# Performance work log

Hardware: AMD Instinct MI355X
Metric: run time of the kernel (lower is better)

The kernel has to match this reference:

```python
import jax, jax.numpy as jnp
import numpy as np
from jax import lax

B, N, C, P = 4, 20000, 21, 100           # batch, anchors, classes (incl. background), proposal_count
SCORE_THR = 0.7
SIGMA = 0.5                              # soft_nms=True -> soft_nms_sigma = 0.5
CLIP_RATIO = 16.0 / 1000.0
BIG = 1e9                                # sentinel for invalid / removed boxes
MAX_RATIO = float(abs(np.log(CLIP_RATIO)))


def setup_inputs() -> dict:
    key = jax.random.key(0)
    k1, k2, k3, k4, k5 = jax.random.split(key, 5)
    score = jax.random.uniform(k1, (B, N, 1), dtype=jnp.float32)
    logits = jax.random.uniform(k2, (B, N, C), dtype=jnp.float32)
    regress = jax.random.normal(k3, (B, N, 4), dtype=jnp.float32) * 0.2
    ctr = jax.random.uniform(k4, (N, 2), minval=0.05, maxval=0.95)
    size = jax.random.uniform(k5, (N, 2), minval=0.02, maxval=0.3)
    anchors = jnp.clip(jnp.concatenate([ctr - 0.5 * size, ctr + 0.5 * size], axis=-1), 0.0, 1.0)
    return {"score": score, "logits": logits, "regress": regress, "anchors": anchors.astype(jnp.float32)}


def _decode(anchors, regress):
    # delta2bbox-style decode (yolo2bbox) with wh-ratio clipping, boxes clipped to [0,1]
    ax1, ay1, ax2, ay2 = anchors[:, 0], anchors[:, 1], anchors[:, 2], anchors[:, 3]
    aw, ah = ax2 - ax1, ay2 - ay1
    acx, acy = ax1 + 0.5 * aw, ay1 + 0.5 * ah
    dx, dy = regress[:, 0], regress[:, 1]
    dw = jnp.clip(regress[:, 2], -MAX_RATIO, MAX_RATIO)
    dh = jnp.clip(regress[:, 3], -MAX_RATIO, MAX_RATIO)
    cx, cy = acx + dx * aw, acy + dy * ah
    w, h = aw * jnp.exp(dw), ah * jnp.exp(dh)
    boxes = jnp.stack([cx - 0.5 * w, cy - 0.5 * h, cx + 0.5 * w, cy + 0.5 * h], axis=-1)
    return jnp.clip(boxes, 0.0, 1.0)


def _iou_one(b, boxes):
    # IoU of one box [4] vs all boxes [N,4]
    x1 = jnp.maximum(b[0], boxes[:, 0])
    y1 = jnp.maximum(b[1], boxes[:, 1])
    x2 = jnp.minimum(b[2], boxes[:, 2])
    y2 = jnp.minimum(b[3], boxes[:, 3])
    inter = jnp.clip(x2 - x1, 0.0) * jnp.clip(y2 - y1, 0.0)
    a = (b[2] - b[0]) * (b[3] - b[1])
    areas = (boxes[:, 2] - boxes[:, 0]) * (boxes[:, 3] - boxes[:, 1])
    return inter / (a + areas - inter + 1e-9)


def _soft_nms(boxes, scores0):
    # Gaussian soft-NMS (TF non_max_suppression_with_scores, soft_nms_sigma>0):
    # weight = exp(-0.5*iou^2/sigma); iou_threshold is ignored in soft mode.
    n = scores0.shape[0]
    ar = jnp.arange(n)

    @jax.checkpoint
    def step(carry, _):
        s, removed = carry
        m = jnp.where(removed, -BIG, s)
        i = jnp.argmax(m)
        valid = m[i] > 0.0
        w = jnp.exp(-0.5 * jnp.square(_iou_one(boxes[i], boxes)) / SIGMA)
        s = jnp.where(valid, s * w, s)
        removed = removed | (ar == i)
        return (s, removed), (i, valid)

    _, (idx, val) = lax.scan(step, (scores0, jnp.zeros(n, bool)), None, length=P)
    return idx, val


def _image(score, logits, regress, anchors):
    le = score * logits                       # [N,C] combined class scores
    label = jnp.argmax(le, axis=-1)
    ms = jnp.max(le, axis=-1)
    valid = (ms >= SCORE_THR) & (label > 0)   # drop background / low score
    boxes = _decode(anchors, regress)         # [N,4]
    cls_scores = jnp.where(valid[None, :], le.T[1:], -BIG)   # [C-1,N]
    idx, val = jax.vmap(_soft_nms, in_axes=(None, 0))(boxes, cls_scores)  # [C-1,P]
    cls = jnp.broadcast_to(jnp.arange(1, C)[:, None], (C - 1, P))
    idx, val, cls = idx.reshape(-1), val.reshape(-1), cls.reshape(-1)
    cand = jnp.where(val, le[idx, cls], -BIG)  # gather_nd on un-decayed logit
    top_s, top_i = lax.top_k(cand, P)          # global top-k over all classes
    fi = idx[top_i]
    ok = (top_s > -BIG / 2)[:, None]
    logit_out = jnp.where(ok, le[fi], 0.0)     # zero-padded like tf.pad
    proposal = jnp.where(ok, boxes[fi], 0.0)
    return logit_out, proposal                 # [P,C], [P,4]


def reference(score, logits, regress, anchors):
    return jax.vmap(_image, in_axes=(0, 0, 0, None))(score, logits, regress, anchors)
```

## Files before the change

kernel.cpp:

```cpp
#include <hip/hip_runtime.h>
#include <climits>
#include <cstdint>

namespace {
constexpr int B = 4, N = 20000, C = 21, P = 100, NC = 20;
constexpr float THR  = 0.7f;
constexpr float BIGF = 1.0e9f;
constexpr float MAXR = 4.135166556742356f;
constexpr float TAU  = 0.8f;
constexpr int NMT  = 512;
constexpr int PCAP = NMT;
constexpr int TKN  = 2048;
constexpr int TKT  = 512;
constexpr int NB   = (N + 255) / 256;
constexpr int GPB  = 2;
constexpr int GB   = (NB + GPB - 1) / GPB;

constexpr size_t OFF_CPACK = 0;
constexpr size_t OFF_MASK  = OFF_CPACK + (size_t)B * N * 32;
constexpr size_t OFF_BCNT  = OFF_MASK  + (size_t)B * N * 4;
constexpr size_t OFF_VCNT  = OFF_BCNT  + 2048;
constexpr size_t OFF_OIDX  = OFF_VCNT  + 64;
constexpr size_t OFF_OVAL  = OFF_OIDX  + (size_t)B * NC * P * 4;
constexpr size_t OFF_OSC   = OFF_OVAL  + (size_t)B * NC * P * 4;
constexpr size_t OFF_OBOX  = OFF_OSC   + (size_t)B * NC * P * 4;
constexpr size_t OFF_SFALL = OFF_OBOX  + (size_t)B * NC * P * 16;
}

template <int CTRL, int RM>
__device__ __forceinline__ float dpp_fmax(float x) {
  int t = __builtin_amdgcn_update_dpp(__float_as_int(x), __float_as_int(x),
                                      CTRL, RM, 0xF, false);
  return fmaxf(x, __int_as_float(t));
}
__device__ __forceinline__ float wave_fmax64(float x) {
  x = dpp_fmax<0x111, 0xF>(x);
  x = dpp_fmax<0x112, 0xF>(x);
  x = dpp_fmax<0x114, 0xF>(x);
  x = dpp_fmax<0x118, 0xF>(x);
  x = dpp_fmax<0x142, 0xA>(x);
  x = dpp_fmax<0x143, 0xC>(x);
  return __int_as_float(__builtin_amdgcn_readlane(__float_as_int(x), 63));
}
__device__ __forceinline__ float fast_rcp(float x) {
  return __builtin_amdgcn_rcpf(x);
}
__device__ __forceinline__ float fast_exp2(float x) {
  return __builtin_amdgcn_exp2f(x);
}
__device__ __forceinline__ unsigned fmap(float v) {
  unsigned u = __float_as_uint(v);
  return (u & 0x80000000u) ? ~u : (u | 0x80000000u);
}
__device__ __forceinline__ float funmap(unsigned u) {
  return __uint_as_float((u & 0x80000000u) ? (u ^ 0x80000000u) : ~u);
}

__global__ __launch_bounds__(256) void k_valid(
    const float* __restrict__ score, const float* __restrict__ logits,
    unsigned* __restrict__ mask, int* __restrict__ bcnt) {
  __shared__ int ws[4];
  int tid = threadIdx.x;
  int n = blockIdx.x * 256 + tid;
  int b = blockIdx.y;
  unsigned mk = 0;
  if (n < N) {
    int bn = b * N + n;
    float sc = score[bn];
    const float* lg = logits + (size_t)bn * C;
    float le[C];
    float ms = -INFINITY;
    int lab = 0;
    #pragma unroll
    for (int c = 0; c < C; ++c) {
      le[c] = __fmul_rn(sc, lg[c]);
      if (le[c] > ms) { ms = le[c]; lab = c; }
    }
    if (ms >= THR && lab > 0) {
      mk = 1u << 20;
      #pragma unroll
      for (int c = 1; c < C; ++c)
        if (le[c] >= TAU) mk |= 1u << (c - 1);
    }
    mask[bn] = mk;
  }
  unsigned long long vb = __ballot(mk != 0);
  if ((tid & 63) == 0) ws[tid >> 6] = __popcll(vb);
  __syncthreads();
  if (tid == 0) bcnt[b * NB + blockIdx.x] = ws[0] + ws[1] + ws[2] + ws[3];
}

__global__ __launch_bounds__(256) void k_compact(
    const float* __restrict__ score, const float* __restrict__ regress,
    const float* __restrict__ anchors, const unsigned* __restrict__ mask,
    const int* __restrict__ bcnt, float* __restrict__ cpack,
    int* __restrict__ vcnt) {
  __shared__ int s_base[4], s_tot[4], s_scan[4];
  int g = blockIdx.x, b = blockIdx.y;
  int tid = threadIdx.x, lane = tid & 63, wid = tid >> 6;
  int idx0 = g * GPB;
  int bv = (tid < idx0) ? bcnt[b * NB + tid] : 0;
  int tv = (tid < NB) ? bcnt[b * NB + tid] : 0;
  #pragma unroll
  for (int off = 32; off; off >>= 1) {
    bv += __shfl_down(bv, off);
    tv += __shfl_down(tv, off);
  }
  if (lane == 0) { s_base[wid] = bv; s_tot[wid] = tv; }
  __syncthreads();
  int base = s_base[0] + s_base[1] + s_base[2] + s_base[3];
  if (g == 0 && tid == 0) vcnt[b] = s_tot[0] + s_tot[1] + s_tot[2] + s_tot[3];

  int n0 = g * (GPB * 256) + tid * GPB;
  unsigned bits = 0; int cnt = 0;
  #pragma unroll
  for (int j = 0; j < GPB; ++j) {
    int n = n0 + j;
    if (n < N && (mask[b * N + n] & (1u << 20))) { bits |= 1u << j; cnt++; }
  }
  int inc = cnt;
  #pragma unroll
  for (int off = 1; off < 64; off <<= 1) {
    int o = __shfl_up(inc, off);
    if (lane >= off) inc += o;
  }
  if (lane == 63) s_scan[wid] = inc;
  __syncthreads();
  int woff = 0;
  for (int k = 0; k < wid; ++k) woff += s_scan[k];
  int pos = base + woff + inc - cnt;
  #pragma unroll
  for (int j = 0; j < GPB; ++j) {
    if (!((bits >> j) & 1u)) continue;
    int n = n0 + j;
    int bn = b * N + n;
    const float* an = anchors + (size_t)n * 4;
    float ax1 = an[0], ay1 = an[1], ax2 = an[2], ay2 = an[3];
    float aw = __fsub_rn(ax2, ax1), ah = __fsub_rn(ay2, ay1);
    float acx = __fadd_rn(ax1, __fmul_rn(0.5f, aw));
    float acy = __fadd_rn(ay1, __fmul_rn(0.5f, ah));
    const float* rg = regress + (size_t)bn * 4;
    float dx = rg[0], dy = rg[1];
    float dw = fminf(fmaxf(rg[2], -MAXR), MAXR);
    float dh = fminf(fmaxf(rg[3], -MAXR), MAXR);
    float cx = __fadd_rn(acx, __fmul_rn(dx, aw));
    float cy = __fadd_rn(acy, __fmul_rn(dy, ah));
    float w = __fmul_rn(aw, expf(dw));
    float h = __fmul_rn(ah, expf(dh));
    float hw = __fmul_rn(0.5f, w), hh = __fmul_rn(0.5f, h);
    float x1 = fminf(fmaxf(__fsub_rn(cx, hw), 0.f), 1.f);
    float y1 = fminf(fmaxf(__fsub_rn(cy, hh), 0.f), 1.f);
    float x2 = fminf(fmaxf(__fadd_rn(cx, hw), 0.f), 1.f);
    float y2 = fminf(fmaxf(__fadd_rn(cy, hh), 0.f), 1.f);
    float area = __fmul_rn(__fsub_rn(x2, x1), __fsub_rn(y2, y1));
    unsigned mk = mask[bn];
    float4* cp = reinterpret_cast<float4*>(cpack) + ((size_t)b * N + pos) * 2;
    cp[0] = make_float4(x1, y1, x2, y2);
    cp[1] = make_float4(__int_as_float(n), score[bn], area, __uint_as_float(mk));
    pos++;
  }
}

__global__ __launch_bounds__(NMT) void k_nms(
    const float* __restrict__ logits, const float* __restrict__ cpack,
    const int* __restrict__ vcnt, float* __restrict__ sfall,
    int* __restrict__ oidx, int* __restrict__ oval,
    float* __restrict__ osc, float* __restrict__ obox) {
  constexpr int NW = NMT / 64;
  __shared__ float4 s_box[PCAP];
  __shared__ float  s_ar[PCAP], s_s[PCAP];
  __shared__ int    s_n[PCAP];
  __shared__ int    s_selj[P];
  __shared__ int    s_wcnt[NW];
  __shared__ int    s_fail;
  __shared__ unsigned long long s_gk[2];
  __shared__ float  s_red[NW];
  __shared__ int    s_redi[NW];

  int blk = blockIdx.x;
  int b = blk / NC;
  int cls = blk % NC + 1;
  int V = vcnt[b];
  int tid = threadIdx.x;
  int lane = tid & 63, wid = tid >> 6;
  const float* cpf = cpack + (size_t)b * N * 8;
  int* oi = oidx + (size_t)blk * P;
  int* ov = oval + (size_t)blk * P;
  float* os = osc + (size_t)blk * P;
  float4* ob = reinterpret_cast<float4*>(obox) + (size_t)blk * P;
  unsigned clsbit = 1u << (cls - 1);

  s_box[tid] = make_float4(0.f, 0.f, 0.f, 0.f);
  if (tid == 0) { s_gk[0] = 0ull; s_gk[1] = 0ull; }

  int ch = (V + NMT - 1) / NMT;
  int v0 = tid * ch, v1 = min(v0 + ch, V);
  int cnt = 0;
  for (int v = v0; v < v1; ++v) {
    unsigned mk = __float_as_uint(cpf[(size_t)v * 8 + 7]);
    if (mk & clsbit) cnt++;
  }
  int inc = cnt;
  #pragma unroll
  for (int off = 1; off < 64; off <<= 1) {
    int o = __shfl_up(inc, off);
    if (lane >= off) inc += o;
  }
  if (lane == 63) s_wcnt[wid] = inc;
  __syncthreads();
  int woff = 0;
  for (int k = 0; k < wid; ++k) woff += s_wcnt[k];
  int pcnt = 0;
  #pragma unroll
  for (int k = 0; k < NW; ++k) pcnt += s_wcnt[k];
  int pos = woff + inc - cnt;
  for (int v = v0; v < v1; ++v) {
    const float4* cp = reinterpret_cast<const float4*>(cpf) + (size_t)v * 2;
    float4 f2 = cp[1];
    unsigned mk = __float_as_uint(f2.w);
    if (mk & clsbit) {
      if (pos < PCAP) {
        float4 f1 = cp[0];
        int n = __float_as_int(f2.x);
        float lg = logits[(size_t)(b * N + n) * C + cls];
        s_s[pos]   = __fmul_rn(f2.y, lg);
        s_box[pos] = f1;
        s_ar[pos]  = f2.z;
        s_n[pos]   = n;
      }
      pos++;
    }
  }
  __syncthreads();

  bool fail0 = (pcnt > PCAP);
  if (!fail0) {
    bool in = tid < pcnt;
    float4 q = s_box[tid];
    float sr = in ? s_s[tid] : -INFINITY;
    float qx = q.x, qy = q.y, qz = q.z, qw = q.w;
    float pa = in ? s_ar[tid] : 0.f;
    unsigned long long kb = 0ull;

    for (int t = 0; t < P; ++t) {
      int par = t & 1;
      float lm = wave_fmax64(sr);
      unsigned long long bm = __ballot(sr == lm);
      int lane_w = __ffsll(bm) - 1;
      if (lane == 0) {
        unsigned inv = 511u - (unsigned)(wid * 64 + lane_w);
        unsigned long long key = ((unsigned long long)(t + 1) << 41) |
                                 ((unsigned long long)fmap(lm) << 9) |
                                 (unsigned long long)inv;
        atomicMax(&s_gk[par], key);
      }
      __syncthreads();
      kb = s_gk[par];
      int j_w = 511 - (int)((unsigned)kb & 511u);
      if (tid == 0) s_selj[t] = j_w;
      float4 wbx = s_box[j_w];
      float wa = __fmul_rn(__fsub_rn(wbx.z, wbx.x),
                           __fsub_rn(wbx.w, wbx.y));
      float s1 = __fadd_rn(wa, 1e-9f);
      float x1 = fmaxf(wbx.x, qx), y1 = fmaxf(wbx.y, qy);
      float x2 = fminf(wbx.z, qz), y2 = fminf(wbx.w, qw);
      float iw = fmaxf(__fsub_rn(x2, x1), 0.f);
      float ih = fmaxf(__fsub_rn(y2, y1), 0.f);
      float inter = __fmul_rn(iw, ih);
      float den = __fsub_rn(__fadd_rn(pa, s1), inter);
      float iou = __fmul_rn(inter, fast_rcp(den));
      float m2 = __fmul_rn(__fmul_rn(iou, iou), -1.44269504089f);
      float wgt = fast_exp2(m2);
      float ns = __fmul_rn(sr, wgt);
      sr = (tid == j_w) ? -INFINITY : ns;
    }
    float gmax = funmap((unsigned)((kb >> 9) & 0xFFFFFFFFull));
    if (tid == 0) s_fail = (gmax < TAU) ? 1 : 0;
    __syncthreads();
    if (!s_fail) {
      if (tid < P) {
        int wj = s_selj[tid];
        oi[tid] = s_n[wj];
        ov[tid] = 1;
        os[tid] = s_s[wj];
        ob[tid] = s_box[wj];
      }
      return;
    }
  }

  __syncthreads();
  float* sg = sfall + (size_t)blk * N;
  for (int v = tid; v < V; v += NMT) {
    const float* c2 = cpf + (size_t)v * 8 + 4;
    int n = __float_as_int(c2[0]);
    sg[v] = __fmul_rn(c2[1], logits[(size_t)(b * N + n) * C + cls]);
  }
  __syncthreads();

  for (int t = 0; t < P; ++t) {
    float bv = -INFINITY; int bi = INT_MAX;
    for (int v = tid; v < V; v += NMT) {
      float sv = sg[v];
      if (sv > bv) { bv = sv; bi = v; }
    }
    #pragma unroll
    for (int off = 32; off; off >>= 1) {
      float ovv = __shfl_down(bv, off); int oii = __shfl_down(bi, off);
      if (ovv > bv || (ovv == bv && oii < bi)) { bv = ovv; bi = oii; }
    }
    if (lane == 0) { s_red[wid] = bv; s_redi[wid] = bi; }
    __syncthreads();
    float wv = -INFINITY; int wi = INT_MAX;
    #pragma unroll
    for (int k = 0; k < NW; ++k) {
      float v = s_red[k]; int i = s_redi[k];
      if (v > wv || (v == wv && i < wi)) { wv = v; wi = i; }
    }
    __syncthreads();
    if (wi == INT_MAX) {
      if (tid == 0) for (int u = t; u < P; ++u) {
        oi[u] = 0; ov[u] = 0; os[u] = 0.f;
        ob[u] = make_float4(0.f, 0.f, 0.f, 0.f);
      }
      break;
    }
    int vd = (wv > 0.0f) ? 1 : 0;
    const float* cw = cpf + (size_t)wi * 8;
    if (tid == 0) {
      int n = __float_as_int(cw[4]);
      oi[t] = n; ov[t] = vd;
      os[t] = __fmul_rn(cw[5], logits[(size_t)(b * N + n) * C + cls]);
      ob[t] = make_float4(cw[0], cw[1], cw[2], cw[3]);
    }
    float w0, w1, w2, w3;
    if (vd) { w0 = cw[0]; w1 = cw[1]; w2 = cw[2]; w3 = cw[3]; }
    else    { w0 = w1 = w2 = w3 = 0.f; }
    float wa = __fmul_rn(__fsub_rn(w2, w0), __fsub_rn(w3, w1));
    for (int v = tid; v < V; v += NMT) {
      float sv = (v == wi) ? -INFINITY : sg[v];
      const float* cq = cpf + (size_t)v * 8;
      float x1 = fmaxf(w0, cq[0]), y1 = fmaxf(w1, cq[1]);
      float x2 = fminf(w2, cq[2]), y2 = fminf(w3, cq[3]);
      float iw = fmaxf(__fsub_rn(x2, x1), 0.f);
      float ih = fmaxf(__fsub_rn(y2, y1), 0.f);
      float inter = __fmul_rn(iw, ih);
      float den = __fadd_rn(__fsub_rn(__fadd_rn(wa, cq[6]), inter), 1e-9f);
      float iou = __fdiv_rn(inter, den);
      float wgt = expf(-__fmul_rn(iou, iou));
      sg[v] = __fmul_rn(sv, wgt);
    }
    __syncthreads();
  }
}

__global__ __launch_bounds__(TKT) void k_topk(
    const float* __restrict__ score, const float* __restrict__ logits,
    const float* __restrict__ obox, const int* __restrict__ oidx,
    const int* __restrict__ oval, const float* __restrict__ osc,
    float* __restrict__ out) {
  __shared__ unsigned long long s_k2[2][TKN];
  __shared__ int s_fi[TKN];

  int b = blockIdx.x;
  int tid = threadIdx.x;
  size_t base = (size_t)b * NC * P;

  unsigned long long v0, v1, v2, v3;
  {
    int j0 = 4 * tid;
    if (j0 + 3 < NC * P) {
      int4   vl4 = *reinterpret_cast<const int4*>(oval + base + j0);
      float4 sc4 = *reinterpret_cast<const float4*>(osc + base + j0);
      int4   fi4 = *reinterpret_cast<const int4*>(oidx + base + j0);
      s_fi[j0]     = fi4.x; s_fi[j0 + 1] = fi4.y;
      s_fi[j0 + 2] = fi4.z; s_fi[j0 + 3] = fi4.w;
      v0 = ((unsigned long long)fmap(vl4.x ? sc4.x : -BIGF) << 32) |
           (unsigned)(~(j0 + 0));
      v1 = ((unsigned long long)fmap(vl4.y ? sc4.y : -BIGF) << 32) |
           (unsigned)(~(j0 + 1));
      v2 = ((unsigned long long)fmap(vl4.z ? sc4.z : -BIGF) << 32) |
           (unsigned)(~(j0 + 2));
      v3 = ((unsigned long long)fmap(vl4.w ? sc4.w : -BIGF) << 32) |
           (unsigned)(~(j0 + 3));
    } else {
      s_fi[j0] = 0; s_fi[j0 + 1] = 0; s_fi[j0 + 2] = 0; s_fi[j0 + 3] = 0;
      unsigned long long hi = (unsigned long long)fmap(-INFINITY) << 32;
      v0 = hi | (unsigned)(~(j0 + 0));
      v1 = hi | (unsigned)(~(j0 + 1));
      v2 = hi | (unsigned)(~(j0 + 2));
      v3 = hi | (unsigned)(~(j0 + 3));
    }
  }

  auto cmpx = [](unsigned long long& a, unsigned long long pv, bool keepmax) {
    bool agt = a > pv;
    a = (keepmax == agt) ? a : pv;
  };
  auto shfl_stage = [&](int k, int j) {
    int xd = j >> 2;
    bool up = ((tid & xd) == 0);
    bool desc = ((tid & (k >> 2)) == 0);
    bool keepmax = (up == desc);
    unsigned long long p0 = __shfl_xor(v0, xd);
    unsigned long long p1 = __shfl_xor(v1, xd);
    unsigned long long p2 = __shfl_xor(v2, xd);
    unsigned long long p3 = __shfl_xor(v3, xd);
    cmpx(v0, p0, keepmax); cmpx(v1, p1, keepmax);
    cmpx(v2, p2, keepmax); cmpx(v3, p3, keepmax);
  };
  auto reg_stage = [&](int k) {
    bool desc = ((tid & (k >> 2)) == 0);
    auto sw = [&](unsigned long long& a, unsigned long long& bb) {
      if (desc ? (a < bb) : (a > bb)) { unsigned long long t = a; a = bb; bb = t; }
    };
    sw(v0, v2); sw(v1, v3);
    sw(v0, v1); sw(v2, v3);
  };
  auto lds_stage = [&](int k, int j, int par) {
    unsigned long long* buf = s_k2[par];
    int j0 = 4 * tid;
    buf[j0] = v0; buf[j0 + 1] = v1; buf[j0 + 2] = v2; buf[j0 + 3] = v3;
    __syncthreads();
    int pj = 4 * (tid ^ (j >> 2));
    unsigned long long p0 = buf[pj], p1 = buf[pj + 1];
    unsigned long long p2 = buf[pj + 2], p3 = buf[pj + 3];
    bool up = ((tid & (j >> 2)) == 0);
    bool desc = ((tid & (k >> 2)) == 0);
    bool keepmax = (up == desc);
    cmpx(v0, p0, keepmax); cmpx(v1, p1, keepmax);
    cmpx(v2, p2, keepmax); cmpx(v3, p3, keepmax);
  };

  { if (v0 < v1) { unsigned long long t = v0; v0 = v1; v1 = t; }
    if (v2 > v3) { unsigned long long t = v2; v2 = v3; v3 = t; } }
  reg_stage(4);
  #pragma unroll
  for (int k = 8; k <= 256; k <<= 1) {
    #pragma unroll
    for (int j = k >> 1; j >= 4; j >>= 1) shfl_stage(k, j);
    reg_stage(k);
  }
  lds_stage(512, 256, 0);
  #pragma unroll
  for (int j = 128; j >= 4; j >>= 1) shfl_stage(512, j);
  reg_stage(512);
  lds_stage(1024, 512, 1);
  lds_stage(1024, 256, 0);
  #pragma unroll
  for (int j = 128; j >= 4; j >>= 1) shfl_stage(1024, j);
  reg_stage(1024);
  lds_stage(2048, 1024, 1);
  lds_stage(2048, 512, 0);
  lds_stage(2048, 256, 1);
  #pragma unroll
  for (int j = 128; j >= 4; j >>= 1) shfl_stage(2048, j);
  reg_stage(2048);

  {
    int j0 = 4 * tid;
    unsigned long long* buf = s_k2[0];
    buf[j0] = v0; buf[j0 + 1] = v1; buf[j0 + 2] = v2; buf[j0 + 3] = v3;
  }
  __syncthreads();
  const unsigned long long* s_key = s_k2[0];

  for (int kk = tid; kk < P * C; kk += TKT) {
    int t = kk / C, cls = kk % C;
    unsigned long long kt = s_key[t];
    float sv = funmap((unsigned)(kt >> 32));
    int j = (int)(~(unsigned)kt);
    bool okp = sv > -BIGF * 0.5f;
    float o = 0.f;
    if (okp) {
      int fi = s_fi[j];
      int bn = b * N + fi;
      o = __fmul_rn(score[bn], logits[(size_t)bn * C + cls]);
    }
    out[((size_t)b * P + t) * C + cls] = o;
  }
  for (int kk = tid; kk < P * 4; kk += TKT) {
    int t = kk / 4, d = kk % 4;
    unsigned long long kt = s_key[t];
    float sv = funmap((unsigned)(kt >> 32));
    int j = (int)(~(unsigned)kt);
    bool okp = sv > -BIGF * 0.5f;
    float o = 0.f;
    if (okp) o = obox[(base + j) * 4 + d];
    out[(size_t)B * P * C + ((size_t)b * P + t) * 4 + d] = o;
  }
}

extern "C" void kernel_launch(void* const* d_in, const int* in_sizes, int n_in,
                              void* d_out, int out_size, void* d_ws, size_t ws_size,
                              hipStream_t stream) {
  const float* score   = (const float*)d_in[0];
  const float* logits  = (const float*)d_in[1];
  const float* regress = (const float*)d_in[2];
  const float* anchors = (const float*)d_in[3];
  float* out = (float*)d_out;

  char* ws = (char*)d_ws;
  float*    cpack = (float*)(ws + OFF_CPACK);
  unsigned* mask  = (unsigned*)(ws + OFF_MASK);
  int*      bcnt  = (int*)(ws + OFF_BCNT);
  int*      vcnt  = (int*)(ws + OFF_VCNT);
  int*      oidx  = (int*)(ws + OFF_OIDX);
  int*      oval  = (int*)(ws + OFF_OVAL);
  float*    osc   = (float*)(ws + OFF_OSC);
  float*    obox  = (float*)(ws + OFF_OBOX);
  float*    sfall = (float*)(ws + OFF_SFALL);

  k_valid<<<dim3(NB, B), 256, 0, stream>>>(score, logits, mask, bcnt);
  k_compact<<<dim3(GB, B), 256, 0, stream>>>(score, regress, anchors, mask,
                                             bcnt, cpack, vcnt);
  k_nms<<<B * NC, NMT, 0, stream>>>(logits, cpack, vcnt, sfall, oidx, oval,
                                    osc, obox);
  k_topk<<<B, TKT, 0, stream>>>(score, logits, obox, oidx, oval, osc, out);
}
```

Measured before the change: 79.17 us.

## Fuse top-k into NMS kernel via last-block atomic counter; vectorize logit loads

The separate top-k kernel is folded into the NMS kernel: each block bumps a per-image done counter after its class finishes, and the last block for each image runs the bitonic top-k using a shared-memory union that reuses the NMS buffers. This removes one kernel launch and its dependency gap. k_valid also reads logits with float4 loads and resets the counters. The risk is that the top-k work now waits on the slowest class block, and correctness relies on threadfence ordering. The logit rows are 84 bytes, so float4 loads are misaligned for rows whose index is not a multiple of 4.

After: 91.15 us. 15.1% more time.

```diff
diff --git a/kernel.cpp b/kernel.cpp
--- a/kernel.cpp
+++ b/kernel.cpp
@@ -11,7 +11,6 @@
 constexpr int NMT  = 512;
 constexpr int PCAP = NMT;
 constexpr int TKN  = 2048;
-constexpr int TKT  = 512;
 constexpr int NB   = (N + 255) / 256;
 constexpr int GPB  = 2;
 constexpr int GB   = (NB + GPB - 1) / GPB;
@@ -20,6 +19,7 @@
 constexpr size_t OFF_MASK  = OFF_CPACK + (size_t)B * N * 32;
 constexpr size_t OFF_BCNT  = OFF_MASK  + (size_t)B * N * 4;
 constexpr size_t OFF_VCNT  = OFF_BCNT  + 2048;
+constexpr size_t OFF_DONE  = OFF_VCNT  + 16;
 constexpr size_t OFF_OIDX  = OFF_VCNT  + 64;
 constexpr size_t OFF_OVAL  = OFF_OIDX  + (size_t)B * NC * P * 4;
 constexpr size_t OFF_OSC   = OFF_OVAL  + (size_t)B * NC * P * 4;
@@ -58,24 +58,33 @@
 
 __global__ __launch_bounds__(256) void k_valid(
     const float* __restrict__ score, const float* __restrict__ logits,
-    unsigned* __restrict__ mask, int* __restrict__ bcnt) {
+    unsigned* __restrict__ mask, int* __restrict__ bcnt,
+    int* __restrict__ done) {
   __shared__ int ws[4];
   int tid = threadIdx.x;
   int n = blockIdx.x * 256 + tid;
   int b = blockIdx.y;
+  if (blockIdx.x == 0 && tid == 0) done[b] = 0;
   unsigned mk = 0;
   if (n < N) {
     int bn = b * N + n;
     float sc = score[bn];
     const float* lg = logits + (size_t)bn * C;
     float le[C];
+    #pragma unroll
+    for (int q = 0; q < 5; ++q) {
+      float4 v4 = *reinterpret_cast<const float4*>(lg + 4 * q);
+      le[4 * q + 0] = __fmul_rn(sc, v4.x);
+      le[4 * q + 1] = __fmul_rn(sc, v4.y);
+      le[4 * q + 2] = __fmul_rn(sc, v4.z);
+      le[4 * q + 3] = __fmul_rn(sc, v4.w);
+    }
+    le[20] = __fmul_rn(sc, lg[20]);
     float ms = -INFINITY;
     int lab = 0;
     #pragma unroll
-    for (int c = 0; c < C; ++c) {
-      le[c] = __fmul_rn(sc, lg[c]);
+    for (int c = 0; c < C; ++c)
       if (le[c] > ms) { ms = le[c]; lab = c; }
-    }
     if (ms >= THR && lab > 0) {
       mk = 1u << 20;
       #pragma unroll
@@ -162,20 +171,41 @@
 }
 
 __global__ __launch_bounds__(NMT) void k_nms(
-    const float* __restrict__ logits, const float* __restrict__ cpack,
-    const int* __restrict__ vcnt, float* __restrict__ sfall,
-    int* __restrict__ oidx, int* __restrict__ oval,
-    float* __restrict__ osc, float* __restrict__ obox) {
+    const float* __restrict__ score, const float* __restrict__ logits,
+    const float* __restrict__ cpack, const int* __restrict__ vcnt,
+    float* __restrict__ sfall, int* __restrict__ oidx,
+    int* __restrict__ oval, float* __restrict__ osc,
+    float* __restrict__ obox, int* __restrict__ done,
+    float* __restrict__ out) {
   constexpr int NW = NMT / 64;
-  __shared__ float4 s_box[PCAP];
-  __shared__ float  s_ar[PCAP], s_s[PCAP];
-  __shared__ int    s_n[PCAP];
-  __shared__ int    s_selj[P];
-  __shared__ int    s_wcnt[NW];
-  __shared__ int    s_fail;
-  __shared__ unsigned long long s_gk[2];
-  __shared__ float  s_red[NW];
-  __shared__ int    s_redi[NW];
+  union ShU {
+    struct {
+      float4 box[PCAP];
+      float  ar[PCAP], s[PCAP];
+      int    n[PCAP];
+      int    selj[P];
+      int    wcnt[NW];
+      unsigned long long gk[2];
+      float  red[NW];
+      int    redi[NW];
+    } nm;
+    struct {
+      unsigned long long k2[2][TKN];
+      int fi[TKN];
+    } tk;
+  };
+  __shared__ ShU sh;
+  __shared__ int s_fail, s_last;
+
+  float4* s_box = sh.nm.box;
+  float*  s_ar  = sh.nm.ar;
+  float*  s_s   = sh.nm.s;
+  int*    s_n   = sh.nm.n;
+  int*    s_selj = sh.nm.selj;
+  int*    s_wcnt = sh.nm.wcnt;
+  unsigned long long* s_gk = sh.nm.gk;
+  float*  s_red = sh.nm.red;
+  int*    s_redi = sh.nm.redi;
 
   int blk = blockIdx.x;
   int b = blk / NC;
@@ -234,6 +264,7 @@
   __syncthreads();
 
   bool fail0 = (pcnt > PCAP);
+  bool okdone = false;
   if (!fail0) {
     bool in = tid < pcnt;
     float4 q = s_box[tid];
@@ -285,88 +316,89 @@
         os[tid] = s_s[wj];
         ob[tid] = s_box[wj];
       }
-      return;
-    }
-  }
-
-  __syncthreads();
-  float* sg = sfall + (size_t)blk * N;
-  for (int v = tid; v < V; v += NMT) {
-    const float* c2 = cpf + (size_t)v * 8 + 4;
-    int n = __float_as_int(c2[0]);
-    sg[v] = __fmul_rn(c2[1], logits[(size_t)(b * N + n) * C + cls]);
-  }
-  __syncthreads();
-
-  for (int t = 0; t < P; ++t) {
-    float bv = -INFINITY; int bi = INT_MAX;
+      okdone = true;
+    }
+  }
+
+  if (!okdone) {
+    __syncthreads();
+    float* sg = sfall + (size_t)blk * N;
     for (int v = tid; v < V; v += NMT) {
-      float sv = sg[v];
-      if (sv > bv) { bv = sv; bi = v; }
-    }
-    #pragma unroll
-    for (int off = 32; off; off >>= 1) {
-      float ovv = __shfl_down(bv, off); int oii = __shfl_down(bi, off);
-      if (ovv > bv || (ovv == bv && oii < bi)) { bv = ovv; bi = oii; }
-    }
-    if (lane == 0) { s_red[wid] = bv; s_redi[wid] = bi; }
+      const float* c2 = cpf + (size_t)v * 8 + 4;
+      int n = __float_as_int(c2[0]);
+      sg[v] = __fmul_rn(c2[1], logits[(size_t)(b * N + n) * C + cls]);
+    }
     __syncthreads();
-    float wv = -INFINITY; int wi = INT_MAX;
-    #pragma unroll
-    for (int k = 0; k < NW; ++k) {
-      float v = s_red[k]; int i = s_redi[k];
-      if (v > wv || (v == wv && i < wi)) { wv = v; wi = i; }
-    }
-    __syncthreads();
-    if (wi == INT_MAX) {
-      if (tid == 0) for (int u = t; u < P; ++u) {
-        oi[u] = 0; ov[u] = 0; os[u] = 0.f;
-        ob[u] = make_float4(0.f, 0.f, 0.f, 0.f);
-      }
-      break;
-    }
-    int vd = (wv > 0.0f) ? 1 : 0;
-    const float* cw = cpf + (size_t)wi * 8;
-    if (tid == 0) {
-      int n = __float_as_int(cw[4]);
-      oi[t] = n; ov[t] = vd;
-      os[t] = __fmul_rn(cw[5], logits[(size_t)(b * N + n) * C + cls]);
-      ob[t] = make_float4(cw[0], cw[1], cw[2], cw[3]);
-    }
-    float w0, w1, w2, w3;
-    if (vd) { w0 = cw[0]; w1 = cw[1]; w2 = cw[2]; w3 = cw[3]; }
-    else    { w0 = w1 = w2 = w3 = 0.f; }
-    float wa = __fmul_rn(__fsub_rn(w2, w0), __fsub_rn(w3, w1));
-    for (int v = tid; v < V; v += NMT) {
-      float sv = (v == wi) ? -INFINITY : sg[v];
-      const float* cq = cpf + (size_t)v * 8;
-      float x1 = fmaxf(w0, cq[0]), y1 = fmaxf(w1, cq[1]);
-      float x2 = fminf(w2, cq[2]), y2 = fminf(w3, cq[3]);
-      float iw = fmaxf(__fsub_rn(x2, x1), 0.f);
-      float ih = fmaxf(__fsub_rn(y2, y1), 0.f);
-      float inter = __fmul_rn(iw, ih);
-      float den = __fadd_rn(__fsub_rn(__fadd_rn(wa, cq[6]), inter), 1e-9f);
-      float iou = __fdiv_rn(inter, den);
-      float wgt = expf(-__fmul_rn(iou, iou));
-      sg[v] = __fmul_rn(sv, wgt);
-    }
-    __syncthreads();
-  }
-}
-
-__global__ __launch_bounds__(TKT) void k_topk(
-    const float* __restrict__ score, const float* __restrict__ logits,
-    const float* __restrict__ obox, const int* __restrict__ oidx,
-    const int* __restrict__ oval, const float* __restrict__ osc,
-    float* __restrict__ out) {
-  __shared__ unsigned long long s_k2[2][TKN];
-  __shared__ int s_fi[TKN];
-
-  int b = blockIdx.x;
-  int tid = threadIdx.x;
+
+    for (int t = 0; t < P; ++t) {
+      float bv = -INFINITY; int bi = INT_MAX;
+      for (int v = tid; v < V; v += NMT) {
+        float sv = sg[v];
+        if (sv > bv) { bv = sv; bi = v; }
+      }
+      #pragma unroll
+      for (int off = 32; off; off >>= 1) {
+        float ovv = __shfl_down(bv, off); int oii = __shfl_down(bi, off);
+        if (ovv > bv || (ovv == bv && oii < bi)) { bv = ovv; bi = oii; }
+      }
+      if (lane == 0) { s_red[wid] = bv; s_redi[wid] = bi; }
+      __syncthreads();
+      float wv = -INFINITY; int wi = INT_MAX;
+      #pragma unroll
+      for (int k = 0; k < NW; ++k) {
+        float v = s_red[k]; int i = s_redi[k];
+        if (v > wv || (v == wv && i < wi)) { wv = v; wi = i; }
+      }
+      __syncthreads();
+      if (wi == INT_MAX) {
+        if (tid == 0) for (int u = t; u < P; ++u) {
+          oi[u] = 0; ov[u] = 0; os[u] = 0.f;
+          ob[u] = make_float4(0.f, 0.f, 0.f, 0.f);
+        }
+        break;
+      }
+      int vd = (wv > 0.0f) ? 1 : 0;
+      const float* cw = cpf + (size_t)wi * 8;
+      if (tid == 0) {
+        int n = __float_as_int(cw[4]);
+        oi[t] = n; ov[t] = vd;
+        os[t] = __fmul_rn(cw[5], logits[(size_t)(b * N + n) * C + cls]);
+        ob[t] = make_float4(cw[0], cw[1], cw[2], cw[3]);
+      }
+      float w0, w1, w2, w3;
+      if (vd) { w0 = cw[0]; w1 = cw[1]; w2 = cw[2]; w3 = cw[3]; }
+      else    { w0 = w1 = w2 = w3 = 0.f; }
+      float wa = __fmul_rn(__fsub_rn(w2, w0), __fsub_rn(w3, w1));
+      for (int v = tid; v < V; v += NMT) {
+        float sv = (v == wi) ? -INFINITY : sg[v];
+        const float* cq = cpf + (size_t)v * 8;
+        float x1 = fmaxf(w0, cq[0]), y1 = fmaxf(w1, cq[1]);
+        float x2 = fminf(w2, cq[2]), y2 = fminf(w3, cq[3]);
+        float iw = fmaxf(__fsub_rn(x2, x1), 0.f);
+        float ih = fmaxf(__fsub_rn(y2, y1), 0.f);
+        float inter = __fmul_rn(iw, ih);
+        float den = __fadd_rn(__fsub_rn(__fadd_rn(wa, cq[6]), inter), 1e-9f);
+        float iou = __fdiv_rn(inter, den);
+        float wgt = expf(-__fmul_rn(iou, iou));
+        sg[v] = __fmul_rn(sv, wgt);
+      }
+      __syncthreads();
+    }
+  }
+
+  __threadfence();
+  __syncthreads();
+  if (tid == 0) s_last = atomicAdd(done + b, 1);
+  __syncthreads();
+  if (s_last != NC - 1) return;
+  __threadfence();
+  __syncthreads();
+
+  unsigned long long (*s_k2)[TKN] = sh.tk.k2;
+  int* s_fi = sh.tk.fi;
   size_t base = (size_t)b * NC * P;
 
-  unsigned long long v0, v1, v2, v3;
+  unsigned long long v0k, v1k, v2k, v3k;
   {
     int j0 = 4 * tid;
     if (j0 + 3 < NC * P) {
@@ -375,21 +407,21 @@
       int4   fi4 = *reinterpret_cast<const int4*>(oidx + base + j0);
       s_fi[j0]     = fi4.x; s_fi[j0 + 1] = fi4.y;
       s_fi[j0 + 2] = fi4.z; s_fi[j0 + 3] = fi4.w;
-      v0 = ((unsigned long long)fmap(vl4.x ? sc4.x : -BIGF) << 32) |
-           (unsigned)(~(j0 + 0));
-      v1 = ((unsigned long long)fmap(vl4.y ? sc4.y : -BIGF) << 32) |
-           (unsigned)(~(j0 + 1));
-      v2 = ((unsigned long long)fmap(vl4.z ? sc4.z : -BIGF) << 32) |
-           (unsigned)(~(j0 + 2));
-      v3 = ((unsigned long long)fmap(vl4.w ? sc4.w : -BIGF) << 32) |
-           (unsigned)(~(j0 + 3));
+      v0k = ((unsigned long long)fmap(vl4.x ? sc4.x : -BIGF) << 32) |
+            (unsigned)(~(j0 + 0));
+      v1k = ((unsigned long long)fmap(vl4.y ? sc4.y : -BIGF) << 32) |
+            (unsigned)(~(j0 + 1));
+      v2k = ((unsigned long long)fmap(vl4.z ? sc4.z : -BIGF) << 32) |
+            (unsigned)(~(j0 + 2));
+      v3k = ((unsigned long long)fmap(vl4.w ? sc4.w : -BIGF) << 32) |
+            (unsigned)(~(j0 + 3));
     } else {
       s_fi[j0] = 0; s_fi[j0 + 1] = 0; s_fi[j0 + 2] = 0; s_fi[j0 + 3] = 0;
       unsigned long long hi = (unsigned long long)fmap(-INFINITY) << 32;
-      v0 = hi | (unsigned)(~(j0 + 0));
-      v1 = hi | (unsigned)(~(j0 + 1));
-      v2 = hi | (unsigned)(~(j0 + 2));
-      v3 = hi | (unsigned)(~(j0 + 3));
+      v0k = hi | (unsigned)(~(j0 + 0));
+      v1k = hi | (unsigned)(~(j0 + 1));
+      v2k = hi | (unsigned)(~(j0 + 2));
+      v3k = hi | (unsigned)(~(j0 + 3));
     }
   }
 
@@ -402,25 +434,25 @@
     bool up = ((tid & xd) == 0);
     bool desc = ((tid & (k >> 2)) == 0);
     bool keepmax = (up == desc);
-    unsigned long long p0 = __shfl_xor(v0, xd);
-    unsigned long long p1 = __shfl_xor(v1, xd);
-    unsigned long long p2 = __shfl_xor(v2, xd);
-    unsigned long long p3 = __shfl_xor(v3, xd);
-    cmpx(v0, p0, keepmax); cmpx(v1, p1, keepmax);
-    cmpx(v2, p2, keepmax); cmpx(v3, p3, keepmax);
+    unsigned long long p0 = __shfl_xor(v0k, xd);
+    unsigned long long p1 = __shfl_xor(v1k, xd);
+    unsigned long long p2 = __shfl_xor(v2k, xd);
+    unsigned long long p3 = __shfl_xor(v3k, xd);
+    cmpx(v0k, p0, keepmax); cmpx(v1k, p1, keepmax);
+    cmpx(v2k, p2, keepmax); cmpx(v3k, p3, keepmax);
   };
   auto reg_stage = [&](int k) {
     bool desc = ((tid & (k >> 2)) == 0);
     auto sw = [&](unsigned long long& a, unsigned long long& bb) {
       if (desc ? (a < bb) : (a > bb)) { unsigned long long t = a; a = bb; bb = t; }
     };
-    sw(v0, v2); sw(v1, v3);
-    sw(v0, v1); sw(v2, v3);
+    sw(v0k, v2k); sw(v1k, v3k);
+    sw(v0k, v1k); sw(v2k, v3k);
   };
   auto lds_stage = [&](int k, int j, int par) {
     unsigned long long* buf = s_k2[par];
     int j0 = 4 * tid;
-    buf[j0] = v0; buf[j0 + 1] = v1; buf[j0 + 2] = v2; buf[j0 + 3] = v3;
+    buf[j0] = v0k; buf[j0 + 1] = v1k; buf[j0 + 2] = v2k; buf[j0 + 3] = v3k;
     __syncthreads();
     int pj = 4 * (tid ^ (j >> 2));
     unsigned long long p0 = buf[pj], p1 = buf[pj + 1];
@@ -428,12 +460,12 @@
     bool up = ((tid & (j >> 2)) == 0);
     bool desc = ((tid & (k >> 2)) == 0);
     bool keepmax = (up == desc);
-    cmpx(v0, p0, keepmax); cmpx(v1, p1, keepmax);
-    cmpx(v2, p2, keepmax); cmpx(v3, p3, keepmax);
+    cmpx(v0k, p0, keepmax); cmpx(v1k, p1, keepmax);
+    cmpx(v2k, p2, keepmax); cmpx(v3k, p3, keepmax);
   };
 
-  { if (v0 < v1) { unsigned long long t = v0; v0 = v1; v1 = t; }
-    if (v2 > v3) { unsigned long long t = v2; v2 = v3; v3 = t; } }
+  { if (v0k < v1k) { unsigned long long t = v0k; v0k = v1k; v1k = t; }
+    if (v2k > v3k) { unsigned long long t = v2k; v2k = v3k; v3k = t; } }
   reg_stage(4);
   #pragma unroll
   for (int k = 8; k <= 256; k <<= 1) {
@@ -460,13 +492,13 @@
   {
     int j0 = 4 * tid;
     unsigned long long* buf = s_k2[0];
-    buf[j0] = v0; buf[j0 + 1] = v1; buf[j0 + 2] = v2; buf[j0 + 3] = v3;
+    buf[j0] = v0k; buf[j0 + 1] = v1k; buf[j0 + 2] = v2k; buf[j0 + 3] = v3k;
   }
   __syncthreads();
   const unsigned long long* s_key = s_k2[0];
 
-  for (int kk = tid; kk < P * C; kk += TKT) {
-    int t = kk / C, cls = kk % C;
+  for (int kk = tid; kk < P * C; kk += NMT) {
+    int t = kk / C, cc = kk % C;
     unsigned long long kt = s_key[t];
     float sv = funmap((unsigned)(kt >> 32));
     int j = (int)(~(unsigned)kt);
@@ -475,11 +507,11 @@
     if (okp) {
       int fi = s_fi[j];
       int bn = b * N + fi;
-      o = __fmul_rn(score[bn], logits[(size_t)bn * C + cls]);
-    }
-    out[((size_t)b * P + t) * C + cls] = o;
-  }
-  for (int kk = tid; kk < P * 4; kk += TKT) {
+      o = __fmul_rn(score[bn], logits[(size_t)bn * C + cc]);
+    }
+    out[((size_t)b * P + t) * C + cc] = o;
+  }
+  for (int kk = tid; kk < P * 4; kk += NMT) {
     int t = kk / 4, d = kk % 4;
     unsigned long long kt = s_key[t];
     float sv = funmap((unsigned)(kt >> 32));
@@ -505,16 +537,16 @@
   unsigned* mask  = (unsigned*)(ws + OFF_MASK);
   int*      bcnt  = (int*)(ws + OFF_BCNT);
   int*      vcnt  = (int*)(ws + OFF_VCNT);
+  int*      done  = (int*)(ws + OFF_DONE);
   int*      oidx  = (int*)(ws + OFF_OIDX);
   int*      oval  = (int*)(ws + OFF_OVAL);
   float*    osc   = (float*)(ws + OFF_OSC);
   float*    obox  = (float*)(ws + OFF_OBOX);
   float*    sfall = (float*)(ws + OFF_SFALL);
 
-  k_valid<<<dim3(NB, B), 256, 0, stream>>>(score, logits, mask, bcnt);
+  k_valid<<<dim3(NB, B), 256, 0, stream>>>(score, logits, mask, bcnt, done);
   k_compact<<<dim3(GB, B), 256, 0, stream>>>(score, regress, anchors, mask,
                                              bcnt, cpack, vcnt);
-  k_nms<<<B * NC, NMT, 0, stream>>>(logits, cpack, vcnt, sfall, oidx, oval,
-                                    osc, obox);
-  k_topk<<<B, TKT, 0, stream>>>(score, logits, obox, oidx, oval, osc, out);
-}
+  k_nms<<<B * NC, NMT, 0, stream>>>(score, logits, cpack, vcnt, sfall, oidx,
+                                    oval, osc, obox, done, out);
+}
```
